# Kernel tuning notes

Hardware: AMD Instinct MI355X
Metric: run time of the kernel (lower is better)

The kernel has to match this reference:

```python
import jax, jax.numpy as jnp
import numpy as np

N_E = 2048
E_DIM = 256
N_TOK = 65536
BETA = 0.25


def setup_inputs() -> dict:
    key = jax.random.key(0)
    k1, k2 = jax.random.split(key)
    z = jax.random.normal(k1, (N_TOK, E_DIM), dtype=jnp.float32)
    # torch init: uniform(-1/n_e, 1/n_e)
    embedding = jax.random.uniform(k2, (N_E, E_DIM), dtype=jnp.float32,
                                   minval=-1.0 / N_E, maxval=1.0 / N_E)
    return {"z": z, "embedding": embedding}


def reference(z, embedding):
    beta = BETA
    # squared L2 distances: ||z||^2 + ||e||^2 - 2 z @ e^T   -> (N, n_e)
    d = (jnp.sum(z * z, axis=1, keepdims=True)
         + jnp.sum(embedding * embedding, axis=1)
         - 2.0 * jnp.matmul(z, embedding.T))
    idx = jnp.argmin(d, axis=1)            # (N,)
    z_q = embedding[idx]                   # gather == one-hot @ E, same math

    sg = jax.lax.stop_gradient
    loss = (beta * jnp.mean((sg(z_q) - z) ** 2)
            + jnp.mean((z_q - sg(z)) ** 2))
    # straight-through estimator
    z_q_st = z + sg(z_q - z)

    # e_mean = column mean of the one-hot matrix == codebook usage histogram / N
    counts = jnp.zeros((embedding.shape[0],), dtype=z.dtype).at[idx].add(1.0)
    e_mean = counts / z.shape[0]
    perplexity = jnp.exp(-jnp.sum(e_mean * jnp.log(e_mean + 1e-10)))

    return z_q_st, loss, perplexity, idx[:, None]
```

## Files before the change

kernel.cpp:

```cpp
#include <hip/hip_runtime.h>
#include <cfloat>
#include <cmath>
#include <cstdint>

#define N_TOK 65536
#define N_E   2048
#define E_DIM 256
#define BETA  0.25

#define MGN 8e-4f
#define CMAX 16

#define WS_LOSSPART 0
#define WS_A        16384
#define WS_B        278528
#define WS_IDXF     286720
#define WS_COUNTS   548864
#define WS_CCNT     2654208
#define WS_CAND     2916352

typedef __attribute__((ext_vector_type(8))) _Float16 half8;
typedef __attribute__((ext_vector_type(4))) float f32x4;

__device__ __forceinline__ ushort f2h(float f) {
  union { _Float16 h; ushort u; } c;
  c.h = (_Float16)f;
  return c.u;
}

__device__ __forceinline__ void gload_lds16(const void* g, void* l) {
  __builtin_amdgcn_global_load_lds(
      (const __attribute__((address_space(1))) unsigned int*)(g),
      (__attribute__((address_space(3))) unsigned int*)(l), 16, 0, 0);
}

__device__ __forceinline__ float4 f4add(float4 x, float4 y) {
  float4 r;
  r.x = __fadd_rn(x.x, y.x); r.y = __fadd_rn(x.y, y.y);
  r.z = __fadd_rn(x.z, y.z); r.w = __fadd_rn(x.w, y.w);
  return r;
}

__device__ __forceinline__ float4 f4shfl_xor(float4 x, int m) {
  float4 r;
  r.x = __shfl_xor(x.x, m, 64);
  r.y = __shfl_xor(x.y, m, 64);
  r.z = __shfl_xor(x.z, m, 64);
  r.w = __shfl_xor(x.w, m, 64);
  return r;
}

__device__ __forceinline__ float chain_m(const float* __restrict__ zp,
                                         const float* __restrict__ ep) {
  float acc = 0.f;
  for (int k = 0; k < E_DIM; k += 4) {
    const float4 zz = *(const float4*)(zp + k);
    const float4 ee = *(const float4*)(ep + k);
    acc = __fmaf_rn(zz.x, ee.x, acc);
    acc = __fmaf_rn(zz.y, ee.y, acc);
    acc = __fmaf_rn(zz.z, ee.z, acc);
    acc = __fmaf_rn(zz.w, ee.w, acc);
  }
  return acc;
}

__global__ __launch_bounds__(256) void k_prep(
    const float* __restrict__ z, const float* __restrict__ E,
    ushort* __restrict__ zf, ushort* __restrict__ ef,
    float* __restrict__ a, float* __restrict__ b, int* __restrict__ counts) {
  if (blockIdx.x == 0) {
    for (int i = threadIdx.x; i < N_E; i += 256) counts[i] = 0;
  }
  const int l = threadIdx.x & 63;
  const int gw = blockIdx.x * 4 + (threadIdx.x >> 6);
  const int NROW = N_TOK + N_E;

  for (int row = gw; row < NROW; row += 2048 * 4) {
    const bool isZ = row < N_TOK;
    const int lr = isZ ? row : row - N_TOK;
    const float* src = (isZ ? z + (size_t)lr * E_DIM : E + (size_t)lr * E_DIM);
    ushort* dst = (isZ ? zf + (size_t)lr * E_DIM : ef + (size_t)lr * E_DIM);
    const float scale = isZ ? 1.0f : 2048.0f;

    const float4 v = *(const float4*)(src + l * 4);
    ushort4 o;
    o.x = f2h(v.x * scale); o.y = f2h(v.y * scale);
    o.z = f2h(v.z * scale); o.w = f2h(v.w * scale);
    *(ushort4*)(dst + l * 4) = o;

    float4 q;
    q.x = __fmul_rn(v.x, v.x); q.y = __fmul_rn(v.y, v.y);
    q.z = __fmul_rn(v.z, v.z); q.w = __fmul_rn(v.w, v.w);

    float4 s1 = f4add(q, f4shfl_xor(q, 4));
    float4 s2 = f4add(s1, f4shfl_xor(s1, 8));
    float4 s3 = f4add(s2, f4shfl_xor(s2, 16));
    float4 u4 = f4add(s3, f4shfl_xor(s3, 2));
    float4 v4 = f4add(u4, f4shfl_xor(u4, 1));
    const float w0 = __fadd_rn(v4.x, v4.z);
    const float w1 = __fadd_rn(v4.y, v4.w);
    const float blk = __fadd_rn(w0, w1);
    const float other = __shfl_xor(blk, 32, 64);
    const float s = __fadd_rn(blk, other);

    if (l == 0) {
      if (isZ) a[lr] = s; else b[lr] = s;
    }
  }
}

__global__ __launch_bounds__(512) void k_mfma(
    const ushort* __restrict__ zf, const ushort* __restrict__ ef,
    const float* __restrict__ b, int* __restrict__ gcnt,
    ushort* __restrict__ gcand) {
  extern __shared__ char sm[];
  int*    s_cnt  = (int*)(sm + 65536);
  ushort* s_idx  = (ushort*)(sm + 66048);
  float*  s_val  = (float*)(sm + 70144);
  float*  s_rmin = (float*)(sm + 78336);

  const int tid = threadIdx.x;
  const int wv  = tid >> 6;
  const int l   = tid & 63;
  const int c16 = l & 15;
  const int kb  = l >> 4;
  const int tokBase = blockIdx.x * 128 + wv * 16;

  if (tid < 128) s_cnt[tid] = 0;

  half8 Az[8];
  {
    const ushort* za = zf + (size_t)(tokBase + c16) * E_DIM + kb * 8;
#pragma unroll
    for (int kk = 0; kk < 8; ++kk) Az[kk] = *(const half8*)(za + kk * 32);
  }

#pragma unroll
  for (int i = 0; i < 4; ++i) {
    const int g = i * 512 + tid;
    const int cg = g >> 9, kk = (g >> 6) & 7;
    const int cs = g & 15, ks = (g >> 4) & 3;
    gload_lds16(ef + (size_t)(cg * 16 + cs) * E_DIM + kk * 32 + ks * 8,
                sm + g * 16);
  }
  __syncthreads();

  float runmin[4] = {FLT_MAX, FLT_MAX, FLT_MAX, FLT_MAX};

  for (int ct = 0; ct < 32; ++ct) {
    const int cur = ct & 1;
    if (ct + 1 < 32) {
      const ushort* panel = ef + (size_t)(ct + 1) * (64 * E_DIM);
      char* dst = sm + (cur ^ 1) * 32768;
#pragma unroll
      for (int i = 0; i < 4; ++i) {
        const int g = i * 512 + tid;
        const int cg = g >> 9, kk = (g >> 6) & 7;
        const int cs = g & 15, ks = (g >> 4) & 3;
        gload_lds16(panel + (size_t)(cg * 16 + cs) * E_DIM + kk * 32 + ks * 8,
                    dst + g * 16);
      }
    }
    float bc[4];
#pragma unroll
    for (int cg = 0; cg < 4; ++cg) bc[cg] = b[ct * 64 + cg * 16 + c16];

    f32x4 acc[4];
#pragma unroll
    for (int cg = 0; cg < 4; ++cg) acc[cg] = (f32x4){0.f, 0.f, 0.f, 0.f};

    const char* lb = sm + cur * 32768;
#pragma unroll
    for (int kk = 0; kk < 8; ++kk) {
      half8 Bf[4];
#pragma unroll
      for (int cg = 0; cg < 4; ++cg)
        Bf[cg] = *(const half8*)(lb + ((((cg << 3) | kk) << 6 | l) << 4));
#pragma unroll
      for (int cg = 0; cg < 4; ++cg)
        acc[cg] = __builtin_amdgcn_mfma_f32_16x16x32_f16(
            Az[kk], Bf[cg], acc[cg], 0, 0, 0);
    }

    float sv[4][4];
#pragma unroll
    for (int cg = 0; cg < 4; ++cg)
#pragma unroll
      for (int r = 0; r < 4; ++r)
        sv[cg][r] = __fmaf_rn(acc[cg][r], -0.0009765625f, bc[cg]);
    float tmin[4];
#pragma unroll
    for (int r = 0; r < 4; ++r)
      tmin[r] = fminf(fminf(sv[0][r], sv[1][r]), fminf(sv[2][r], sv[3][r]));
#pragma unroll
    for (int m = 1; m < 16; m <<= 1)
#pragma unroll
      for (int r = 0; r < 4; ++r)
        tmin[r] = fminf(tmin[r], __shfl_xor(tmin[r], m, 64));
    float thr[4];
    bool anyc = false;
#pragma unroll
    for (int r = 0; r < 4; ++r) {
      runmin[r] = fminf(runmin[r], tmin[r]);
      thr[r] = runmin[r] + MGN;
    }
#pragma unroll
    for (int cg = 0; cg < 4; ++cg)
#pragma unroll
      for (int r = 0; r < 4; ++r) anyc |= (sv[cg][r] <= thr[r]);
    if (__any(anyc)) {
#pragma unroll
      for (int cg = 0; cg < 4; ++cg)
#pragma unroll
        for (int r = 0; r < 4; ++r)
          if (sv[cg][r] <= thr[r]) {
            const int tokl = wv * 16 + kb * 4 + r;
            const int p = atomicAdd(&s_cnt[tokl], 1);
            if (p < CMAX) {
              s_idx[tokl * CMAX + p] = (ushort)(ct * 64 + cg * 16 + c16);
              s_val[tokl * CMAX + p] = sv[cg][r];
            }
          }
    }
    __syncthreads();
  }

  if (c16 == 0) {
#pragma unroll
    for (int r = 0; r < 4; ++r)
      s_rmin[wv * 16 + kb * 4 + r] = runmin[r];
  }
  __syncthreads();

  if (tid < 128) {
    const int t = blockIdx.x * 128 + tid;
    const int cnt = s_cnt[tid];
    if (cnt > CMAX) {
      gcnt[t] = 1000;
    } else {
      const float thr = s_rmin[tid] + MGN;
      int nk = 0;
      for (int p = 0; p < cnt; ++p)
        if (s_val[tid * CMAX + p] <= thr)
          gcand[(size_t)t * CMAX + nk++] = s_idx[tid * CMAX + p];
      gcnt[t] = nk;
    }
  }
}

__global__ __launch_bounds__(256) void k_refine(
    const float* __restrict__ z, const float* __restrict__ E,
    const float* __restrict__ a, const float* __restrict__ b,
    const int* __restrict__ gcnt, const ushort* __restrict__ gcand,
    int* __restrict__ idxF, float* __restrict__ out_idx,
    int* __restrict__ counts) {
  const int t = blockIdx.x * 256 + threadIdx.x;
  if (t >= N_TOK) return;
  const int cnt = gcnt[t];
  if (cnt > CMAX) return;
  int bestj;
  if (cnt == 1) {
    bestj = gcand[(size_t)t * CMAX];
  } else {
    float bv = FLT_MAX;
    int bj = 1 << 30;
    const float* zp = z + (size_t)t * E_DIM;
    for (int p = 0; p < cnt; ++p) {
      const int c = gcand[(size_t)t * CMAX + p];
      const float m = chain_m(zp, E + (size_t)c * E_DIM);
      const float D = __fsub_rn(__fadd_rn(a[t], b[c]), __fmul_rn(2.0f, m));
      if (D < bv || (D == bv && c < bj)) { bv = D; bj = c; }
    }
    bestj = bj;
  }
  idxF[t] = bestj;
  out_idx[t] = (float)bestj;
  atomicAdd(&counts[bestj], 1);
}

__global__ __launch_bounds__(256) void k_fallback(
    const float* __restrict__ z, const float* __restrict__ E,
    const float* __restrict__ a, const float* __restrict__ b,
    const int* __restrict__ gcnt, int* __restrict__ idxF,
    float* __restrict__ out_idx, int* __restrict__ counts) {
  __shared__ float rv[256];
  __shared__ int ri[256];
  const int t0 = blockIdx.x * 64;
  for (int t = t0; t < t0 + 64; ++t) {
    if (gcnt[t] <= CMAX) continue;
    const float* zp = z + (size_t)t * E_DIM;
    float bv = FLT_MAX;
    int bj = 1 << 30;
    for (int c = threadIdx.x; c < N_E; c += 256) {
      const float m = chain_m(zp, E + (size_t)c * E_DIM);
      const float D = __fsub_rn(__fadd_rn(a[t], b[c]), __fmul_rn(2.0f, m));
      if (D < bv || (D == bv && c < bj)) { bv = D; bj = c; }
    }
    rv[threadIdx.x] = bv;
    ri[threadIdx.x] = bj;
    __syncthreads();
    for (int s = 128; s; s >>= 1) {
      if (threadIdx.x < s) {
        const float ov = rv[threadIdx.x + s];
        const int oj = ri[threadIdx.x + s];
        if (ov < rv[threadIdx.x] ||
            (ov == rv[threadIdx.x] && oj < ri[threadIdx.x])) {
          rv[threadIdx.x] = ov;
          ri[threadIdx.x] = oj;
        }
      }
      __syncthreads();
    }
    if (threadIdx.x == 0) {
      idxF[t] = ri[0];
      out_idx[t] = (float)ri[0];
      atomicAdd(&counts[ri[0]], 1);
    }
    __syncthreads();
  }
}

__global__ __launch_bounds__(256) void k_gather(
    const float* __restrict__ z, const float* __restrict__ E,
    const int* __restrict__ idxF, float* __restrict__ out0,
    double* __restrict__ lossPart) {
  double ls = 0.0;
  const int NU = N_TOK * (E_DIM / 4);
  for (int u = blockIdx.x * 256 + threadIdx.x; u < NU; u += 2048 * 256) {
    const int tok = u >> 6;
    const int d4 = (u & 63) * 4;
    const int c = idxF[tok];
    const float4 zq = *(const float4*)&E[(size_t)c * E_DIM + d4];
    const float4 zv = *(const float4*)&z[(size_t)tok * E_DIM + d4];
    float4 o;
    o.x = __fadd_rn(zv.x, __fsub_rn(zq.x, zv.x));
    o.y = __fadd_rn(zv.y, __fsub_rn(zq.y, zv.y));
    o.z = __fadd_rn(zv.z, __fsub_rn(zq.z, zv.z));
    o.w = __fadd_rn(zv.w, __fsub_rn(zq.w, zv.w));
    *(float4*)&out0[(size_t)u * 4] = o;
    double dx;
    dx = (double)zq.x - (double)zv.x; ls += dx * dx;
    dx = (double)zq.y - (double)zv.y; ls += dx * dx;
    dx = (double)zq.z - (double)zv.z; ls += dx * dx;
    dx = (double)zq.w - (double)zv.w; ls += dx * dx;
  }
  __shared__ double red[256];
  red[threadIdx.x] = ls;
  __syncthreads();
  for (int s = 128; s; s >>= 1) {
    if (threadIdx.x < s) red[threadIdx.x] += red[threadIdx.x + s];
    __syncthreads();
  }
  if (threadIdx.x == 0) lossPart[blockIdx.x] = red[0];
}

__global__ __launch_bounds__(256) void k_final(
    const double* __restrict__ lossPart, const int* __restrict__ counts,
    float* __restrict__ outLoss, float* __restrict__ outPerp) {
  __shared__ double rs[256], rh[256];
  double s = 0.0, h = 0.0;
  for (int j = threadIdx.x; j < 2048; j += 256) s += lossPart[j];
  for (int j = threadIdx.x; j < N_E; j += 256) {
    const double p = (double)counts[j] * (1.0 / (double)N_TOK);
    h -= p * log(p + 1e-10);
  }
  rs[threadIdx.x] = s;
  rh[threadIdx.x] = h;
  __syncthreads();
  for (int m = 128; m; m >>= 1) {
    if (threadIdx.x < m) {
      rs[threadIdx.x] += rs[threadIdx.x + m];
      rh[threadIdx.x] += rh[threadIdx.x + m];
    }
    __syncthreads();
  }
  if (threadIdx.x == 0) {
    outLoss[0] = (float)((1.0 + BETA) * rs[0] / (double)((size_t)N_TOK * E_DIM));
    outPerp[0] = (float)exp(rh[0]);
  }
}

extern "C" void kernel_launch(void* const* d_in, const int* in_sizes, int n_in,
                              void* d_out, int out_size, void* d_ws, size_t ws_size,
                              hipStream_t stream) {
  const float* z = (const float*)d_in[0];
  const float* E = (const float*)d_in[1];

  float* out0 = (float*)d_out;
  float* outLoss = out0 + (size_t)N_TOK * E_DIM;
  float* outPerp = outLoss + 1;
  float* outIdx = outPerp + 1;

  char* ws = (char*)d_ws;
  double* lossPart = (double*)(ws + WS_LOSSPART);
  float* a = (float*)(ws + WS_A);
  float* b = (float*)(ws + WS_B);
  int* idxF = (int*)(ws + WS_IDXF);
  int* counts = (int*)(ws + WS_COUNTS);
  int* gcnt = (int*)(ws + WS_CCNT);
  ushort* gcand = (ushort*)(ws + WS_CAND);

  ushort* zf = (ushort*)out0;
  ushort* ef = zf + (size_t)N_TOK * E_DIM;

  (void)hipFuncSetAttribute(reinterpret_cast<const void*>(k_mfma),
                            hipFuncAttributeMaxDynamicSharedMemorySize, 78848);

  hipLaunchKernelGGL(k_prep, dim3(2048), dim3(256), 0, stream,
                     z, E, zf, ef, a, b, counts);
  hipLaunchKernelGGL(k_mfma, dim3(N_TOK / 128), dim3(512), 78848, stream,
                     zf, ef, b, gcnt, gcand);
  hipLaunchKernelGGL(k_refine, dim3(N_TOK / 256), dim3(256), 0, stream,
                     z, E, a, b, gcnt, gcand, idxF, outIdx, counts);
  hipLaunchKernelGGL(k_fallback, dim3(N_TOK / 64), dim3(256), 0, stream,
                     z, E, a, b, gcnt, idxF, outIdx, counts);
  hipLaunchKernelGGL(k_gather, dim3(2048), dim3(256), 0, stream,
                     z, E, idxF, out0, lossPart);
  hipLaunchKernelGGL(k_final, dim3(1), dim3(256), 0, stream,
                     lossPart, counts, outLoss, outPerp);
}
```

Measured before the change: 268.1 us.

## Fuse refine into gather kernel and batch the row-min shuffle reduction

The candidate-refinement kernel is merged into the gather/loss kernel, so each block first resolves the best code for its 128 tokens into shared memory and then writes z_q and the loss partials. This removes one launch and the round trip of idxF through global memory. In the MFMA loop the 16-lane shuffle min-reduction now runs only on odd tiles (and the first), with a per-lane partial min used for the threshold on the tiles in between, which reduces cross-lane traffic but can admit more candidates. The fallback kernel is reordered to run before the fused kernel and now covers 512 tokens per block, so it launches fewer blocks.

```diff
diff --git a/kernel.cpp b/kernel.cpp
--- a/kernel.cpp
+++ b/kernel.cpp
@@ -146,6 +146,7 @@
   __syncthreads();
 
   float runmin[4] = {FLT_MAX, FLT_MAX, FLT_MAX, FLT_MAX};
+  float pmin[4]   = {FLT_MAX, FLT_MAX, FLT_MAX, FLT_MAX};
 
   for (int ct = 0; ct < 32; ++ct) {
     const int cur = ct & 1;
@@ -188,26 +189,32 @@
 #pragma unroll
       for (int r = 0; r < 4; ++r)
         sv[cg][r] = __fmaf_rn(acc[cg][r], -0.0009765625f, bc[cg]);
-    float tmin[4];
 #pragma unroll
     for (int r = 0; r < 4; ++r)
-      tmin[r] = fminf(fminf(sv[0][r], sv[1][r]), fminf(sv[2][r], sv[3][r]));
-#pragma unroll
-    for (int m = 1; m < 16; m <<= 1)
-#pragma unroll
-      for (int r = 0; r < 4; ++r)
-        tmin[r] = fminf(tmin[r], __shfl_xor(tmin[r], m, 64));
+      pmin[r] = fminf(pmin[r],
+                      fminf(fminf(sv[0][r], sv[1][r]),
+                            fminf(sv[2][r], sv[3][r])));
+    const bool doB = (ct == 0) || (ct & 1);
+    if (doB) {
+#pragma unroll
+      for (int m = 1; m < 16; m <<= 1)
+#pragma unroll
+        for (int r = 0; r < 4; ++r)
+          pmin[r] = fminf(pmin[r], __shfl_xor(pmin[r], m, 64));
+#pragma unroll
+      for (int r = 0; r < 4; ++r) {
+        runmin[r] = fminf(runmin[r], pmin[r]);
+        pmin[r] = FLT_MAX;
+      }
+    }
     float thr[4];
     bool anyc = false;
 #pragma unroll
     for (int r = 0; r < 4; ++r) {
-      runmin[r] = fminf(runmin[r], tmin[r]);
-      thr[r] = runmin[r] + MGN;
-    }
-#pragma unroll
-    for (int cg = 0; cg < 4; ++cg)
-#pragma unroll
-      for (int r = 0; r < 4; ++r) anyc |= (sv[cg][r] <= thr[r]);
+      thr[r] = fminf(runmin[r], pmin[r]) + MGN;
+#pragma unroll
+      for (int cg = 0; cg < 4; ++cg) anyc |= (sv[cg][r] <= thr[r]);
+    }
     if (__any(anyc)) {
 #pragma unroll
       for (int cg = 0; cg < 4; ++cg)
@@ -248,36 +255,6 @@
   }
 }
 
-__global__ __launch_bounds__(256) void k_refine(
-    const float* __restrict__ z, const float* __restrict__ E,
-    const float* __restrict__ a, const float* __restrict__ b,
-    const int* __restrict__ gcnt, const ushort* __restrict__ gcand,
-    int* __restrict__ idxF, float* __restrict__ out_idx,
-    int* __restrict__ counts) {
-  const int t = blockIdx.x * 256 + threadIdx.x;
-  if (t >= N_TOK) return;
-  const int cnt = gcnt[t];
-  if (cnt > CMAX) return;
-  int bestj;
-  if (cnt == 1) {
-    bestj = gcand[(size_t)t * CMAX];
-  } else {
-    float bv = FLT_MAX;
-    int bj = 1 << 30;
-    const float* zp = z + (size_t)t * E_DIM;
-    for (int p = 0; p < cnt; ++p) {
-      const int c = gcand[(size_t)t * CMAX + p];
-      const float m = chain_m(zp, E + (size_t)c * E_DIM);
-      const float D = __fsub_rn(__fadd_rn(a[t], b[c]), __fmul_rn(2.0f, m));
-      if (D < bv || (D == bv && c < bj)) { bv = D; bj = c; }
-    }
-    bestj = bj;
-  }
-  idxF[t] = bestj;
-  out_idx[t] = (float)bestj;
-  atomicAdd(&counts[bestj], 1);
-}
-
 __global__ __launch_bounds__(256) void k_fallback(
     const float* __restrict__ z, const float* __restrict__ E,
     const float* __restrict__ a, const float* __restrict__ b,
@@ -285,8 +262,8 @@
     float* __restrict__ out_idx, int* __restrict__ counts) {
   __shared__ float rv[256];
   __shared__ int ri[256];
-  const int t0 = blockIdx.x * 64;
-  for (int t = t0; t < t0 + 64; ++t) {
+  const int t0 = blockIdx.x * 512;
+  for (int t = t0; t < t0 + 512; ++t) {
     if (gcnt[t] <= CMAX) continue;
     const float* zp = z + (size_t)t * E_DIM;
     float bv = FLT_MAX;
@@ -320,38 +297,77 @@
   }
 }
 
-__global__ __launch_bounds__(256) void k_gather(
+__global__ __launch_bounds__(256) void k_refgather(
     const float* __restrict__ z, const float* __restrict__ E,
-    const int* __restrict__ idxF, float* __restrict__ out0,
+    const float* __restrict__ a, const float* __restrict__ b,
+    const int* __restrict__ gcnt, const ushort* __restrict__ gcand,
+    int* __restrict__ idxF, float* __restrict__ out_idx,
+    int* __restrict__ counts, float* __restrict__ out0,
     double* __restrict__ lossPart) {
+  __shared__ int s_bj[128];
+  __shared__ double red[256];
+  const int tid = threadIdx.x;
+  const int t0 = blockIdx.x * 128;
+
+  if (tid < 128) {
+    const int t = t0 + tid;
+    const int cnt = gcnt[t];
+    int bestj;
+    if (cnt > CMAX) {
+      bestj = idxF[t];
+    } else if (cnt == 1) {
+      bestj = gcand[(size_t)t * CMAX];
+      idxF[t] = bestj;
+      out_idx[t] = (float)bestj;
+      atomicAdd(&counts[bestj], 1);
+    } else {
+      float bv = FLT_MAX;
+      int bj = 1 << 30;
+      const float* zp = z + (size_t)t * E_DIM;
+      for (int p = 0; p < cnt; ++p) {
+        const int c = gcand[(size_t)t * CMAX + p];
+        const float m = chain_m(zp, E + (size_t)c * E_DIM);
+        const float D = __fsub_rn(__fadd_rn(a[t], b[c]), __fmul_rn(2.0f, m));
+        if (D < bv || (D == bv && c < bj)) { bv = D; bj = c; }
+      }
+      bestj = bj;
+      idxF[t] = bestj;
+      out_idx[t] = (float)bestj;
+      atomicAdd(&counts[bestj], 1);
+    }
+    s_bj[tid] = bestj;
+  }
+  __syncthreads();
+
   double ls = 0.0;
-  const int NU = N_TOK * (E_DIM / 4);
-  for (int u = blockIdx.x * 256 + threadIdx.x; u < NU; u += 2048 * 256) {
-    const int tok = u >> 6;
+#pragma unroll 4
+  for (int i = 0; i < 32; ++i) {
+    const int u = i * 256 + tid;
+    const int tl = u >> 6;
     const int d4 = (u & 63) * 4;
-    const int c = idxF[tok];
+    const int c = s_bj[tl];
+    const size_t tok = (size_t)t0 + tl;
     const float4 zq = *(const float4*)&E[(size_t)c * E_DIM + d4];
-    const float4 zv = *(const float4*)&z[(size_t)tok * E_DIM + d4];
+    const float4 zv = *(const float4*)&z[tok * E_DIM + d4];
     float4 o;
     o.x = __fadd_rn(zv.x, __fsub_rn(zq.x, zv.x));
     o.y = __fadd_rn(zv.y, __fsub_rn(zq.y, zv.y));
     o.z = __fadd_rn(zv.z, __fsub_rn(zq.z, zv.z));
     o.w = __fadd_rn(zv.w, __fsub_rn(zq.w, zv.w));
-    *(float4*)&out0[(size_t)u * 4] = o;
+    *(float4*)&out0[tok * E_DIM + d4] = o;
     double dx;
     dx = (double)zq.x - (double)zv.x; ls += dx * dx;
     dx = (double)zq.y - (double)zv.y; ls += dx * dx;
     dx = (double)zq.z - (double)zv.z; ls += dx * dx;
     dx = (double)zq.w - (double)zv.w; ls += dx * dx;
   }
-  __shared__ double red[256];
-  red[threadIdx.x] = ls;
+  red[tid] = ls;
   __syncthreads();
   for (int s = 128; s; s >>= 1) {
-    if (threadIdx.x < s) red[threadIdx.x] += red[threadIdx.x + s];
+    if (tid < s) red[tid] += red[tid + s];
     __syncthreads();
   }
-  if (threadIdx.x == 0) lossPart[blockIdx.x] = red[0];
+  if (tid == 0) lossPart[blockIdx.x] = red[0];
 }
 
 __global__ __launch_bounds__(256) void k_final(
@@ -359,7 +375,7 @@
     float* __restrict__ outLoss, float* __restrict__ outPerp) {
   __shared__ double rs[256], rh[256];
   double s = 0.0, h = 0.0;
-  for (int j = threadIdx.x; j < 2048; j += 256) s += lossPart[j];
+  for (int j = threadIdx.x; j < 512; j += 256) s += lossPart[j];
   for (int j = threadIdx.x; j < N_E; j += 256) {
     const double p = (double)counts[j] * (1.0 / (double)N_TOK);
     h -= p * log(p + 1e-10);
@@ -410,12 +426,11 @@
                      z, E, zf, ef, a, b, counts);
   hipLaunchKernelGGL(k_mfma, dim3(N_TOK / 128), dim3(512), 78848, stream,
                      zf, ef, b, gcnt, gcand);
-  hipLaunchKernelGGL(k_refine, dim3(N_TOK / 256), dim3(256), 0, stream,
-                     z, E, a, b, gcnt, gcand, idxF, outIdx, counts);
-  hipLaunchKernelGGL(k_fallback, dim3(N_TOK / 64), dim3(256), 0, stream,
+  hipLaunchKernelGGL(k_fallback, dim3(N_TOK / 512), dim3(256), 0, stream,
                      z, E, a, b, gcnt, idxF, outIdx, counts);
-  hipLaunchKernelGGL(k_gather, dim3(2048), dim3(256), 0, stream,
-                     z, E, idxF, out0, lossPart);
+  hipLaunchKernelGGL(k_refgather, dim3(N_TOK / 128), dim3(256), 0, stream,
+                     z, E, a, b, gcnt, gcand, idxF, outIdx, counts, out0,
+                     lossPart);
   hipLaunchKernelGGL(k_final, dim3(1), dim3(256), 0, stream,
                      lossPart, counts, outLoss, outPerp);
 }
```

Result: slower. 326.9 us (+22.0%).
